# Kernel optimization log

Hardware: AMD Instinct MI355X
Metric: run time of the kernel (lower is better)

The kernel has to match this reference:

```python
import jax, jax.numpy as jnp
import numpy as np

EP = 1e-4
MAX_ITER = 100
L = [512, 512]          # context lengths
C = 256                 # padded feature dim == total_dim
HEADS = 2


def nonsat_activation(x, ep=EP, max_iter=MAX_ITER):
    # Fixed-point iteration y <- (2y^3/3 + x)/(y^2+1), y0 = x.
    # Matches torch version: iterate on detached values, final update uses live x.
    xd = jax.lax.stop_gradient(x)
    f = lambda y: (2.0 * y ** 3 / 3.0 + xd) / (y ** 2 + 1.0)

    def cond(s):
        y, y_new, i = s
        return jnp.logical_and(jnp.mean(jnp.abs(y_new - y)) > ep, i <= max_iter)

    def body(s):
        y, y_new, i = s
        return (y_new, f(y_new), i + 1)

    y_prev, _, _ = jax.lax.while_loop(cond, body, (xd, f(xd), 0))
    y_prev = jax.lax.stop_gradient(y_prev)
    # final (returned) update, differentiable w.r.t. x only
    return (2.0 * y_prev ** 3 / 3.0 + x) / (y_prev ** 2 + 1.0)


def setup_inputs() -> dict:
    key = jax.random.key(0)
    k1, k2, k3 = jax.random.split(key, 3)
    x1 = jax.random.normal(k1, (32, 512, 256), dtype=jnp.float32)
    x2 = jax.random.normal(k2, (32, 512, 192), dtype=jnp.float32)
    # xavier_normal_ for U: std = sqrt(2/(fan_in+fan_out)) = sqrt(2/512) = 1/16
    U = jax.random.normal(k3, (HEADS, C, C), dtype=jnp.float32) * (1.0 / 16.0)
    return {"x1": x1, "x2": x2, "U": U}


def reference(x1, x2, U):
    # pad contexts to common feature dim C (zeros on the right)
    contexts = [x1, jnp.pad(x2, ((0, 0), (0, 0), (0, C - x2.shape[-1])))]
    q = sum(L)
    scaling = C ** (-0.5)
    M = jnp.concatenate(contexts, axis=1)  # (B, q, C)

    # mask uses sizes = L[1:] with blocks starting at offset 0 (faithful quirk)
    mask_mul = jnp.ones((q, q), dtype=jnp.float32).at[:L[1], :L[1]].set(0.0)

    h_reps = []
    mask_add = None
    for h in range(HEADS):
        # K[b,i,j] = sum_{c,d} M[b,i,c] U[h,c,d] M[b,j,d]
        K = jnp.einsum('bic,cd,bjd->bij', M, U[h], M) * scaling
        K = nonsat_activation(K)
        if mask_add is None:  # cached after head 0, reused for later heads
            mask_add = jnp.zeros((q, q), dtype=jnp.float32).at[:L[1], :L[1]].set(jnp.min(K))
        K_hat = K * mask_mul + mask_add
        cols = jnp.max(K_hat, axis=1)   # (B, q) max over rows per column
        rows = jnp.max(K_hat, axis=2)   # (B, q) max over cols per row
        alpha = rows + cols             # (B, q)
        reps = []
        offset = 0
        for i, Ci in enumerate(contexts):
            a = alpha[:, offset:offset + L[i]]          # (B, l_i)
            offset += L[i]
            wt = jax.nn.softmax(a, axis=1)              # (B, l_i)
            r = jnp.einsum('bl,blc->bc', wt, Ci)        # (B, C)
            reps.append(r)
        h_reps.append(jnp.stack(reps, axis=1))          # (B, N, C)
    return jnp.stack(h_reps, axis=0)                    # (heads, B, N, C)
```

## Files before the change

kernel.cpp:

```cpp
#include <hip/hip_runtime.h>
#include <math.h>

typedef _Float16 h16;
typedef h16  h16x8 __attribute__((ext_vector_type(8)));
typedef h16  h16x4 __attribute__((ext_vector_type(4)));
typedef float f32x4 __attribute__((ext_vector_type(4)));

#define MH_OFF   ((size_t)0)
#define ML_OFF   (MH_OFF + 16777216)
#define UHT_OFF  (ML_OFF + 16777216)
#define ULT_OFF  (UHT_OFF + 262144)
#define RMA_OFF  (ULT_OFF + 262144)
#define RMH_OFF  (RMA_OFF + 262144)
#define PCM_OFF  (RMH_OFF + 262144)
#define PMIN_OFF (PCM_OFF + 4194304)
#define M0_OFF   (PMIN_OFF + 4096)
#define AL_OFF   (M0_OFF + 16)

__device__ __forceinline__ void glds16(const void* g, void* l) {
    __builtin_amdgcn_global_load_lds(
        (const __attribute__((address_space(1))) unsigned int*)g,
        (__attribute__((address_space(3))) unsigned int*)l, 16, 0, 0);
}

__device__ __forceinline__ float nonsat(float x) {
    float y = x;
#pragma unroll
    for (int i = 0; i < 24; ++i) {
        float y2 = y * y;
        y = fmaf(0.66666667f * y, y2, x) / (y2 + 1.0f);
    }
    return y;
}

__global__ void k_prep(const float* __restrict__ x1, const float* __restrict__ x2,
                       const float* __restrict__ U, h16* __restrict__ MH,
                       h16* __restrict__ ML, h16* __restrict__ UHt,
                       h16* __restrict__ ULt) {
    const int gid = blockIdx.x * 256 + threadIdx.x;
    if (blockIdx.x < 8192) {
        const int g  = gid;
        const int d4 = (g & 63) * 4;
        const int j  = (g >> 6) & 1023;
        const int b  = g >> 16;
        float v[4];
        if (j < 512) {
            const float* p = x1 + ((size_t)(b * 512 + j) * 256 + d4);
#pragma unroll
            for (int k = 0; k < 4; ++k) v[k] = p[k];
        } else {
            const float* p = x2 + (size_t)(b * 512 + (j - 512)) * 192;
#pragma unroll
            for (int k = 0; k < 4; ++k) {
                const int c = d4 + k;
                v[k] = (c < 192) ? p[c] : 0.0f;
            }
        }
        h16x4 hh, ll;
#pragma unroll
        for (int k = 0; k < 4; ++k) {
            const h16 hi = (h16)v[k];
            hh[k] = hi;
            ll[k] = (h16)(v[k] - (float)hi);
        }
        const size_t o = (size_t)g * 4;
        *(h16x4*)&MH[o] = hh;
        *(h16x4*)&ML[o] = ll;
    } else {
        const int g = gid - 8192 * 256;
        if (g < 32768) {
            const int c4 = (g & 63) * 4;
            const int d  = (g >> 6) & 255;
            const int h  = g >> 14;
            h16x4 hh, ll;
#pragma unroll
            for (int k = 0; k < 4; ++k) {
                const float v = U[((size_t)h * 256 + c4 + k) * 256 + d] * 4.0f;
                const h16 hi = (h16)v;
                hh[k] = hi;
                ll[k] = (h16)(v - (float)hi);
            }
            const size_t o = ((size_t)h * 256 + d) * 256 + c4;
            *(h16x4*)&UHt[o] = hh;
            *(h16x4*)&ULt[o] = ll;
        }
    }
}

__global__ __launch_bounds__(256, 2)
void k_main(const h16* __restrict__ MH, const h16* __restrict__ ML,
            const h16* __restrict__ UHt, const h16* __restrict__ ULt,
            float* __restrict__ rmax_all, float* __restrict__ rmax_hi,
            float* __restrict__ pcm, float* __restrict__ pmin) {
    __shared__ __align__(16) h16 sP[2][64 * 256];
    __shared__ __align__(16) h16 sB[256 * 32];

    const int blk  = blockIdx.x;
    const int rblk = blk & 15;
    const int hb   = blk >> 4;
    const int b    = hb & 31;
    const int h    = hb >> 5;
    const int r0   = rblk * 64;
    const int t    = threadIdx.x;
    const int w    = t >> 6;
    const int l    = t & 63;
    const int q    = l >> 4;
    const int ln   = l & 15;
    const int lrow = l >> 2;
    const int lcol = (l & 3) * 8;

    {
        h16* sA = (h16*)sP;
        f32x4 acc[4][4];
        const f32x4 z4 = {0.f, 0.f, 0.f, 0.f};
#pragma unroll
        for (int i = 0; i < 4; ++i)
#pragma unroll
            for (int j = 0; j < 4; ++j) acc[i][j] = z4;

        for (int ch = 0; ch < 24; ++ch) {
            const int term = ch >> 3;
            const int c0   = (ch & 7) * 32;
            const h16* As = (term == 1) ? ML : MH;
            const h16* Bs = (term == 2) ? ULt : UHt;
            __syncthreads();
            glds16(As + ((size_t)(b * 1024 + r0 + w * 16 + lrow) * 256 + c0 + lcol),
                   &sA[(w * 16) * 32]);
#pragma unroll
            for (int p = 0; p < 4; ++p)
                glds16(Bs + ((size_t)(h * 256 + w * 64 + p * 16 + lrow) * 256 + c0 + lcol),
                       &sB[(w * 64 + p * 16) * 32]);
            __syncthreads();
            h16x8 af[4], bf[4];
#pragma unroll
            for (int ti = 0; ti < 4; ++ti)
                af[ti] = *(const h16x8*)&sA[(ti * 16 + ln) * 32 + q * 8];
#pragma unroll
            for (int tj = 0; tj < 4; ++tj)
                bf[tj] = *(const h16x8*)&sB[(w * 64 + tj * 16 + ln) * 32 + q * 8];
#pragma unroll
            for (int ti = 0; ti < 4; ++ti)
#pragma unroll
                for (int tj = 0; tj < 4; ++tj)
                    acc[ti][tj] = __builtin_amdgcn_mfma_f32_16x16x32_f16(
                        af[ti], bf[tj], acc[ti][tj], 0, 0, 0);
        }
        __syncthreads();
#pragma unroll
        for (int ti = 0; ti < 4; ++ti)
#pragma unroll
            for (int tj = 0; tj < 4; ++tj)
#pragma unroll
                for (int reg = 0; reg < 4; ++reg) {
                    const int r = ti * 16 + q * 4 + reg;
                    const int d = w * 64 + tj * 16 + ln;
                    const float v = acc[ti][tj][reg];
                    const h16 hi = (h16)v;
                    const h16 lo = (h16)(v - (float)hi);
                    const int off = r * 256 + (((d >> 3) ^ (r & 7)) << 3) + (d & 7);
                    sP[0][off] = hi;
                    sP[1][off] = lo;
                }
    }
    __syncthreads();

    float rA[16], rH[16];
#pragma unroll
    for (int i = 0; i < 16; ++i) { rA[i] = -INFINITY; rH[i] = -INFINITY; }
    float gmin = INFINITY;

    for (int jt = 0; jt < 4; ++jt) {
        const int j0 = jt * 256;
        f32x4 acc[4][4];
        const f32x4 z4 = {0.f, 0.f, 0.f, 0.f};
#pragma unroll
        for (int i = 0; i < 4; ++i)
#pragma unroll
            for (int j = 0; j < 4; ++j) acc[i][j] = z4;

        for (int ch = 0; ch < 24; ++ch) {
            const int term = ch >> 3;
            const int kc   = ch & 7;
            const int d0   = kc * 32;
            const h16* Bs  = (term == 2) ? ML : MH;
            const h16* sPs = (term == 1) ? sP[1] : sP[0];
            __syncthreads();
#pragma unroll
            for (int p = 0; p < 4; ++p)
                glds16(Bs + ((size_t)(b * 1024 + j0 + w * 64 + p * 16 + lrow) * 256 + d0 + lcol),
                       &sB[(w * 64 + p * 16) * 32]);
            __syncthreads();
            h16x8 af[4], bf[4];
#pragma unroll
            for (int ti = 0; ti < 4; ++ti) {
                const int r = ti * 16 + ln;
                const int g = (kc * 4 + q) ^ (r & 7);
                af[ti] = *(const h16x8*)&sPs[r * 256 + g * 8];
            }
#pragma unroll
            for (int tj = 0; tj < 4; ++tj)
                bf[tj] = *(const h16x8*)&sB[(w * 64 + tj * 16 + ln) * 32 + q * 8];
#pragma unroll
            for (int ti = 0; ti < 4; ++ti)
#pragma unroll
                for (int tj = 0; tj < 4; ++tj)
                    acc[ti][tj] = __builtin_amdgcn_mfma_f32_16x16x32_f16(
                        af[ti], bf[tj], acc[ti][tj], 0, 0, 0);
        }

        const bool hij = (jt >= 2);
#pragma unroll
        for (int ti = 0; ti < 4; ++ti)
#pragma unroll
            for (int reg = 0; reg < 4; ++reg) {
                float m = acc[ti][0][reg];
                m = fmaxf(m, acc[ti][1][reg]);
                m = fmaxf(m, acc[ti][2][reg]);
                m = fmaxf(m, acc[ti][3][reg]);
                const int idx = ti * 4 + reg;
                rA[idx] = fmaxf(rA[idx], m);
                if (hij) rH[idx] = fmaxf(rH[idx], m);
            }
#pragma unroll
        for (int ti = 0; ti < 4; ++ti)
#pragma unroll
            for (int tj = 0; tj < 4; ++tj)
#pragma unroll
                for (int reg = 0; reg < 4; ++reg)
                    gmin = fminf(gmin, acc[ti][tj][reg]);
#pragma unroll
        for (int tj = 0; tj < 4; ++tj) {
            float m = -INFINITY;
#pragma unroll
            for (int ti = 0; ti < 4; ++ti)
#pragma unroll
                for (int reg = 0; reg < 4; ++reg) m = fmaxf(m, acc[ti][tj][reg]);
            m = fmaxf(m, __shfl_xor(m, 16));
            m = fmaxf(m, __shfl_xor(m, 32));
            if (q == 0)
                pcm[(size_t)(hb * 16 + rblk) * 1024 + j0 + w * 64 + tj * 16 + ln] =
                    m * 0.015625f;
        }
    }

#pragma unroll
    for (int off = 1; off < 64; off <<= 1) gmin = fminf(gmin, __shfl_xor(gmin, off));

    __syncthreads();
    float* red = (float*)sB;
#pragma unroll
    for (int ti = 0; ti < 4; ++ti)
#pragma unroll
        for (int reg = 0; reg < 4; ++reg) {
            const int idx = ti * 4 + reg;
            float a = rA[idx], hh = rH[idx];
#pragma unroll
            for (int o2 = 1; o2 < 16; o2 <<= 1) {
                a  = fmaxf(a,  __shfl_xor(a,  o2));
                hh = fmaxf(hh, __shfl_xor(hh, o2));
            }
            if (ln == 0) {
                const int row = ti * 16 + q * 4 + reg;
                red[w * 64 + row]       = a;
                red[256 + w * 64 + row] = hh;
            }
        }
    if (l == 0) red[512 + w] = gmin;
    __syncthreads();
    if (t < 64) {
        const float a  = fmaxf(fmaxf(red[t], red[64 + t]),
                               fmaxf(red[128 + t], red[192 + t]));
        const float hh = fmaxf(fmaxf(red[256 + t], red[320 + t]),
                               fmaxf(red[384 + t], red[448 + t]));
        rmax_all[(size_t)hb * 1024 + r0 + t] = a * 0.015625f;
        rmax_hi [(size_t)hb * 1024 + r0 + t] = hh * 0.015625f;
    }
    if (t == 0)
        pmin[blk] = fminf(fminf(red[512], red[513]),
                          fminf(red[514], red[515])) * 0.015625f;
}

__global__ void k_min(const float* __restrict__ pmin, float* __restrict__ m0) {
    __shared__ float s[4];
    const int t = threadIdx.x;
    float v = fminf(pmin[t], pmin[t + 256]);
#pragma unroll
    for (int off = 1; off < 64; off <<= 1) v = fminf(v, __shfl_xor(v, off));
    if ((t & 63) == 0) s[t >> 6] = v;
    __syncthreads();
    if (t == 0) m0[0] = fminf(fminf(s[0], s[1]), fminf(s[2], s[3]));
}

__global__ void k_alpha(const float* __restrict__ rmax_all,
                        const float* __restrict__ rmax_hi,
                        const float* __restrict__ pcm,
                        const float* __restrict__ m0p,
                        float* __restrict__ alpha) {
    const int hb = blockIdx.x;
    const float m0 = m0p[0];
    for (int it = 0; it < 4; ++it) {
        const int i = it * 256 + threadIdx.x;
        const float rraw = (i < 512) ? fmaxf(m0, rmax_hi[(size_t)hb * 1024 + i])
                                     : rmax_all[(size_t)hb * 1024 + i];
        float call = -INFINITY, chi = -INFINITY;
#pragma unroll
        for (int rb = 0; rb < 16; ++rb) {
            const float v = pcm[(size_t)(hb * 16 + rb) * 1024 + i];
            call = fmaxf(call, v);
            if (rb >= 8) chi = fmaxf(chi, v);
        }
        const float craw = (i < 512) ? fmaxf(m0, chi) : call;
        alpha[(size_t)hb * 1024 + i] = nonsat(rraw) + nonsat(craw);
    }
}

__global__ __launch_bounds__(256)
void k_out(const float* __restrict__ alpha, const float* __restrict__ x1,
           const float* __restrict__ x2, float* __restrict__ out) {
    __shared__ float wv[512];
    __shared__ float sm[4], ss[4];
    const int blk = blockIdx.x;
    const int seg = blk & 1;
    const int hb  = blk >> 1;
    const int b   = hb & 31;
    const int t   = threadIdx.x;
    const float* ap = alpha + (size_t)hb * 1024 + seg * 512;
    const float a0 = ap[t], a1 = ap[t + 256];

    float m = fmaxf(a0, a1);
#pragma unroll
    for (int off = 1; off < 64; off <<= 1) m = fmaxf(m, __shfl_xor(m, off));
    if ((t & 63) == 0) sm[t >> 6] = m;
    __syncthreads();
    const float amax = fmaxf(fmaxf(sm[0], sm[1]), fmaxf(sm[2], sm[3]));

    const float e0 = __expf(a0 - amax), e1 = __expf(a1 - amax);
    wv[t] = e0; wv[t + 256] = e1;
    float s = e0 + e1;
#pragma unroll
    for (int off = 1; off < 64; off <<= 1) s += __shfl_xor(s, off);
    if ((t & 63) == 0) ss[t >> 6] = s;
    __syncthreads();
    const float inv = 1.0f / (ss[0] + ss[1] + ss[2] + ss[3]);

    float acc = 0.0f;
    if (seg == 0) {
        const float* xp = x1 + (size_t)b * 512 * 256 + t;
#pragma unroll 4
        for (int l = 0; l < 512; ++l) acc = fmaf(wv[l], xp[(size_t)l * 256], acc);
        out[blk * 256 + t] = acc * inv;
    } else {
        if (t < 192) {
            const float* xp = x2 + (size_t)b * 512 * 192 + t;
#pragma unroll 4
            for (int l = 0; l < 512; ++l) acc = fmaf(wv[l], xp[(size_t)l * 192], acc);
            out[blk * 256 + t] = acc * inv;
        } else {
            out[blk * 256 + t] = 0.0f;
        }
    }
}

extern "C" void kernel_launch(void* const* d_in, const int* in_sizes, int n_in,
                              void* d_out, int out_size, void* d_ws, size_t ws_size,
                              hipStream_t stream) {
    const float* x1 = (const float*)d_in[0];
    const float* x2 = (const float*)d_in[1];
    const float* U  = (const float*)d_in[2];
    float* out = (float*)d_out;
    char* wsb  = (char*)d_ws;

    h16*   MHp  = (h16*)(wsb + MH_OFF);
    h16*   MLp  = (h16*)(wsb + ML_OFF);
    h16*   UHt  = (h16*)(wsb + UHT_OFF);
    h16*   ULt  = (h16*)(wsb + ULT_OFF);
    float* rma  = (float*)(wsb + RMA_OFF);
    float* rmh  = (float*)(wsb + RMH_OFF);
    float* pcm  = (float*)(wsb + PCM_OFF);
    float* pmin = (float*)(wsb + PMIN_OFF);
    float* m0   = (float*)(wsb + M0_OFF);
    float* al   = (float*)(wsb + AL_OFF);

    hipLaunchKernelGGL(k_prep,  dim3(8320), dim3(256), 0, stream, x1, x2, U,
                       MHp, MLp, UHt, ULt);
    hipLaunchKernelGGL(k_main,  dim3(1024), dim3(256), 0, stream, MHp, MLp,
                       UHt, ULt, rma, rmh, pcm, pmin);
    hipLaunchKernelGGL(k_min,   dim3(1),    dim3(256), 0, stream, pmin, m0);
    hipLaunchKernelGGL(k_alpha, dim3(64),   dim3(256), 0, stream, rma, rmh, pcm, m0, al);
    hipLaunchKernelGGL(k_out,   dim3(128),  dim3(256), 0, stream, al, x1, x2, out);
}
```

Measured before the change: 315.4 us.

## Load GEMM fragments directly from global, fuse min/alpha into main and output kernels

Both GEMM stages in k_main now load MFMA fragments straight from global memory into registers, without the global-to-LDS staging and the barrier pairs around it. The three split-precision terms now run inside one k-loop. The second GEMM uses wider per-wave tiles (4x8 fragments covering 512 columns per pass), and row maxima are reduced with shuffles into shared memory. The global minimum is computed with an integer-keyed atomicMin, restricted to head 0 blocks, and this replaces the separate k_min kernel. The alpha computation is folded into the output kernel, which removes two launches and an intermediate buffer, at the cost of uncoalesced 16-byte global reads and higher register pressure.

```diff
diff --git a/kernel.cpp b/kernel.cpp
--- a/kernel.cpp
+++ b/kernel.cpp
@@ -13,15 +13,7 @@
 #define RMA_OFF  (ULT_OFF + 262144)
 #define RMH_OFF  (RMA_OFF + 262144)
 #define PCM_OFF  (RMH_OFF + 262144)
-#define PMIN_OFF (PCM_OFF + 4194304)
-#define M0_OFF   (PMIN_OFF + 4096)
-#define AL_OFF   (M0_OFF + 16)
-
-__device__ __forceinline__ void glds16(const void* g, void* l) {
-    __builtin_amdgcn_global_load_lds(
-        (const __attribute__((address_space(1))) unsigned int*)g,
-        (__attribute__((address_space(3))) unsigned int*)l, 16, 0, 0);
-}
+#define M0_OFF   (PCM_OFF + 4194304)
 
 __device__ __forceinline__ float nonsat(float x) {
     float y = x;
@@ -33,10 +25,18 @@
     return y;
 }
 
+__device__ __forceinline__ int fkey(float f) {
+    const int i = __float_as_int(f);
+    return (i >= 0) ? i : (i ^ 0x7fffffff);
+}
+__device__ __forceinline__ float funkey(int k) {
+    return __int_as_float((k >= 0) ? k : (k ^ 0x7fffffff));
+}
+
 __global__ void k_prep(const float* __restrict__ x1, const float* __restrict__ x2,
                        const float* __restrict__ U, h16* __restrict__ MH,
                        h16* __restrict__ ML, h16* __restrict__ UHt,
-                       h16* __restrict__ ULt) {
+                       h16* __restrict__ ULt, int* __restrict__ m0key) {
     const int gid = blockIdx.x * 256 + threadIdx.x;
     if (blockIdx.x < 8192) {
         const int g  = gid;
@@ -83,6 +83,8 @@
             const size_t o = ((size_t)h * 256 + d) * 256 + c4;
             *(h16x4*)&UHt[o] = hh;
             *(h16x4*)&ULt[o] = ll;
+        } else if (g == 32768) {
+            *m0key = 0x7fffffff;
         }
     }
 }
@@ -91,9 +93,9 @@
 void k_main(const h16* __restrict__ MH, const h16* __restrict__ ML,
             const h16* __restrict__ UHt, const h16* __restrict__ ULt,
             float* __restrict__ rmax_all, float* __restrict__ rmax_hi,
-            float* __restrict__ pcm, float* __restrict__ pmin) {
+            float* __restrict__ pcm, int* __restrict__ m0key) {
     __shared__ __align__(16) h16 sP[2][64 * 256];
-    __shared__ __align__(16) h16 sB[256 * 32];
+    __shared__ float red[512 + 4];
 
     const int blk  = blockIdx.x;
     const int rblk = blk & 15;
@@ -106,11 +108,8 @@
     const int l    = t & 63;
     const int q    = l >> 4;
     const int ln   = l & 15;
-    const int lrow = l >> 2;
-    const int lcol = (l & 3) * 8;
 
     {
-        h16* sA = (h16*)sP;
         f32x4 acc[4][4];
         const f32x4 z4 = {0.f, 0.f, 0.f, 0.f};
 #pragma unroll
@@ -118,34 +117,42 @@
 #pragma unroll
             for (int j = 0; j < 4; ++j) acc[i][j] = z4;
 
-        for (int ch = 0; ch < 24; ++ch) {
-            const int term = ch >> 3;
-            const int c0   = (ch & 7) * 32;
-            const h16* As = (term == 1) ? ML : MH;
-            const h16* Bs = (term == 2) ? ULt : UHt;
-            __syncthreads();
-            glds16(As + ((size_t)(b * 1024 + r0 + w * 16 + lrow) * 256 + c0 + lcol),
-                   &sA[(w * 16) * 32]);
-#pragma unroll
-            for (int p = 0; p < 4; ++p)
-                glds16(Bs + ((size_t)(h * 256 + w * 64 + p * 16 + lrow) * 256 + c0 + lcol),
-                       &sB[(w * 64 + p * 16) * 32]);
-            __syncthreads();
-            h16x8 af[4], bf[4];
+        for (int kc = 0; kc < 8; ++kc) {
+            const int c0 = kc * 32;
+            h16x8 aH[4], aL[4], bH[4], bL[4];
+#pragma unroll
+            for (int ti = 0; ti < 4; ++ti) {
+                const size_t off =
+                    (size_t)(b * 1024 + r0 + ti * 16 + ln) * 256 + c0 + q * 8;
+                aH[ti] = *(const h16x8*)&MH[off];
+                aL[ti] = *(const h16x8*)&ML[off];
+            }
+#pragma unroll
+            for (int tj = 0; tj < 4; ++tj) {
+                const size_t off =
+                    (size_t)(h * 256 + w * 64 + tj * 16 + ln) * 256 + c0 + q * 8;
+                bH[tj] = *(const h16x8*)&UHt[off];
+                bL[tj] = *(const h16x8*)&ULt[off];
+            }
 #pragma unroll
             for (int ti = 0; ti < 4; ++ti)
-                af[ti] = *(const h16x8*)&sA[(ti * 16 + ln) * 32 + q * 8];
-#pragma unroll
-            for (int tj = 0; tj < 4; ++tj)
-                bf[tj] = *(const h16x8*)&sB[(w * 64 + tj * 16 + ln) * 32 + q * 8];
+#pragma unroll
+                for (int tj = 0; tj < 4; ++tj)
+                    acc[ti][tj] = __builtin_amdgcn_mfma_f32_16x16x32_f16(
+                        aH[ti], bH[tj], acc[ti][tj], 0, 0, 0);
 #pragma unroll
             for (int ti = 0; ti < 4; ++ti)
 #pragma unroll
                 for (int tj = 0; tj < 4; ++tj)
                     acc[ti][tj] = __builtin_amdgcn_mfma_f32_16x16x32_f16(
-                        af[ti], bf[tj], acc[ti][tj], 0, 0, 0);
-        }
-        __syncthreads();
+                        aL[ti], bH[tj], acc[ti][tj], 0, 0, 0);
+#pragma unroll
+            for (int ti = 0; ti < 4; ++ti)
+#pragma unroll
+                for (int tj = 0; tj < 4; ++tj)
+                    acc[ti][tj] = __builtin_amdgcn_mfma_f32_16x16x32_f16(
+                        aH[ti], bL[tj], acc[ti][tj], 0, 0, 0);
+        }
 #pragma unroll
         for (int ti = 0; ti < 4; ++ti)
 #pragma unroll
@@ -164,72 +171,71 @@
     }
     __syncthreads();
 
-    float rA[16], rH[16];
-#pragma unroll
-    for (int i = 0; i < 16; ++i) { rA[i] = -INFINITY; rH[i] = -INFINITY; }
     float gmin = INFINITY;
 
-    for (int jt = 0; jt < 4; ++jt) {
-        const int j0 = jt * 256;
-        f32x4 acc[4][4];
+    for (int jt = 0; jt < 2; ++jt) {
+        const int jbase = jt * 512 + w * 128;
+        f32x4 acc[4][8];
         const f32x4 z4 = {0.f, 0.f, 0.f, 0.f};
 #pragma unroll
         for (int i = 0; i < 4; ++i)
 #pragma unroll
-            for (int j = 0; j < 4; ++j) acc[i][j] = z4;
-
-        for (int ch = 0; ch < 24; ++ch) {
-            const int term = ch >> 3;
-            const int kc   = ch & 7;
-            const int d0   = kc * 32;
-            const h16* Bs  = (term == 2) ? ML : MH;
-            const h16* sPs = (term == 1) ? sP[1] : sP[0];
-            __syncthreads();
-#pragma unroll
-            for (int p = 0; p < 4; ++p)
-                glds16(Bs + ((size_t)(b * 1024 + j0 + w * 64 + p * 16 + lrow) * 256 + d0 + lcol),
-                       &sB[(w * 64 + p * 16) * 32]);
-            __syncthreads();
-            h16x8 af[4], bf[4];
+            for (int j = 0; j < 8; ++j) acc[i][j] = z4;
+
+        for (int kc = 0; kc < 8; ++kc) {
+            const int d0 = kc * 32;
+            h16x8 aH[4], aL[4], bb[8];
 #pragma unroll
             for (int ti = 0; ti < 4; ++ti) {
                 const int r = ti * 16 + ln;
                 const int g = (kc * 4 + q) ^ (r & 7);
-                af[ti] = *(const h16x8*)&sPs[r * 256 + g * 8];
-            }
-#pragma unroll
-            for (int tj = 0; tj < 4; ++tj)
-                bf[tj] = *(const h16x8*)&sB[(w * 64 + tj * 16 + ln) * 32 + q * 8];
-#pragma unroll
-            for (int ti = 0; ti < 4; ++ti)
-#pragma unroll
-                for (int tj = 0; tj < 4; ++tj)
-                    acc[ti][tj] = __builtin_amdgcn_mfma_f32_16x16x32_f16(
-                        af[ti], bf[tj], acc[ti][tj], 0, 0, 0);
-        }
-
-        const bool hij = (jt >= 2);
+                aH[ti] = *(const h16x8*)&sP[0][r * 256 + g * 8];
+                aL[ti] = *(const h16x8*)&sP[1][r * 256 + g * 8];
+            }
+#pragma unroll
+            for (int tj = 0; tj < 8; ++tj)
+                bb[tj] = *(const h16x8*)&MH[
+                    (size_t)(b * 1024 + jbase + tj * 16 + ln) * 256 + d0 + q * 8];
+#pragma unroll
+            for (int tj = 0; tj < 8; ++tj)
+#pragma unroll
+                for (int ti = 0; ti < 4; ++ti)
+                    acc[ti][tj] = __builtin_amdgcn_mfma_f32_16x16x32_f16(
+                        aH[ti], bb[tj], acc[ti][tj], 0, 0, 0);
+#pragma unroll
+            for (int tj = 0; tj < 8; ++tj)
+#pragma unroll
+                for (int ti = 0; ti < 4; ++ti)
+                    acc[ti][tj] = __builtin_amdgcn_mfma_f32_16x16x32_f16(
+                        aL[ti], bb[tj], acc[ti][tj], 0, 0, 0);
+#pragma unroll
+            for (int tj = 0; tj < 8; ++tj)
+                bb[tj] = *(const h16x8*)&ML[
+                    (size_t)(b * 1024 + jbase + tj * 16 + ln) * 256 + d0 + q * 8];
+#pragma unroll
+            for (int tj = 0; tj < 8; ++tj)
+#pragma unroll
+                for (int ti = 0; ti < 4; ++ti)
+                    acc[ti][tj] = __builtin_amdgcn_mfma_f32_16x16x32_f16(
+                        aH[ti], bb[tj], acc[ti][tj], 0, 0, 0);
+        }
+
 #pragma unroll
         for (int ti = 0; ti < 4; ++ti)
 #pragma unroll
             for (int reg = 0; reg < 4; ++reg) {
                 float m = acc[ti][0][reg];
-                m = fmaxf(m, acc[ti][1][reg]);
-                m = fmaxf(m, acc[ti][2][reg]);
-                m = fmaxf(m, acc[ti][3][reg]);
-                const int idx = ti * 4 + reg;
-                rA[idx] = fmaxf(rA[idx], m);
-                if (hij) rH[idx] = fmaxf(rH[idx], m);
-            }
-#pragma unroll
-        for (int ti = 0; ti < 4; ++ti)
-#pragma unroll
-            for (int tj = 0; tj < 4; ++tj)
-#pragma unroll
-                for (int reg = 0; reg < 4; ++reg)
-                    gmin = fminf(gmin, acc[ti][tj][reg]);
-#pragma unroll
-        for (int tj = 0; tj < 4; ++tj) {
+#pragma unroll
+                for (int tj = 1; tj < 8; ++tj) m = fmaxf(m, acc[ti][tj][reg]);
+                m = fmaxf(m, __shfl_xor(m, 1));
+                m = fmaxf(m, __shfl_xor(m, 2));
+                m = fmaxf(m, __shfl_xor(m, 4));
+                m = fmaxf(m, __shfl_xor(m, 8));
+                if (ln == 0)
+                    red[(jt * 4 + w) * 64 + ti * 16 + q * 4 + reg] = m;
+            }
+#pragma unroll
+        for (int tj = 0; tj < 8; ++tj) {
             float m = -INFINITY;
 #pragma unroll
             for (int ti = 0; ti < 4; ++ti)
@@ -238,85 +244,47 @@
             m = fmaxf(m, __shfl_xor(m, 16));
             m = fmaxf(m, __shfl_xor(m, 32));
             if (q == 0)
-                pcm[(size_t)(hb * 16 + rblk) * 1024 + j0 + w * 64 + tj * 16 + ln] =
+                pcm[(size_t)(hb * 16 + rblk) * 1024 + jbase + tj * 16 + ln] =
                     m * 0.015625f;
         }
+#pragma unroll
+        for (int ti = 0; ti < 4; ++ti)
+#pragma unroll
+            for (int tj = 0; tj < 8; ++tj)
+#pragma unroll
+                for (int reg = 0; reg < 4; ++reg)
+                    gmin = fminf(gmin, acc[ti][tj][reg]);
     }
 
 #pragma unroll
     for (int off = 1; off < 64; off <<= 1) gmin = fminf(gmin, __shfl_xor(gmin, off));
-
-    __syncthreads();
-    float* red = (float*)sB;
-#pragma unroll
-    for (int ti = 0; ti < 4; ++ti)
-#pragma unroll
-        for (int reg = 0; reg < 4; ++reg) {
-            const int idx = ti * 4 + reg;
-            float a = rA[idx], hh = rH[idx];
-#pragma unroll
-            for (int o2 = 1; o2 < 16; o2 <<= 1) {
-                a  = fmaxf(a,  __shfl_xor(a,  o2));
-                hh = fmaxf(hh, __shfl_xor(hh, o2));
-            }
-            if (ln == 0) {
-                const int row = ti * 16 + q * 4 + reg;
-                red[w * 64 + row]       = a;
-                red[256 + w * 64 + row] = hh;
-            }
-        }
     if (l == 0) red[512 + w] = gmin;
     __syncthreads();
+
     if (t < 64) {
-        const float a  = fmaxf(fmaxf(red[t], red[64 + t]),
-                               fmaxf(red[128 + t], red[192 + t]));
-        const float hh = fmaxf(fmaxf(red[256 + t], red[320 + t]),
-                               fmaxf(red[384 + t], red[448 + t]));
-        rmax_all[(size_t)hb * 1024 + r0 + t] = a * 0.015625f;
+        float a = -INFINITY, hh = -INFINITY;
+#pragma unroll
+        for (int w2 = 0; w2 < 4; ++w2) {
+            a  = fmaxf(a,  red[w2 * 64 + t]);
+            const float v1 = red[(4 + w2) * 64 + t];
+            a  = fmaxf(a, v1);
+            hh = fmaxf(hh, v1);
+        }
+        rmax_all[(size_t)hb * 1024 + r0 + t] = a  * 0.015625f;
         rmax_hi [(size_t)hb * 1024 + r0 + t] = hh * 0.015625f;
     }
-    if (t == 0)
-        pmin[blk] = fminf(fminf(red[512], red[513]),
-                          fminf(red[514], red[515])) * 0.015625f;
-}
-
-__global__ void k_min(const float* __restrict__ pmin, float* __restrict__ m0) {
-    __shared__ float s[4];
-    const int t = threadIdx.x;
-    float v = fminf(pmin[t], pmin[t + 256]);
-#pragma unroll
-    for (int off = 1; off < 64; off <<= 1) v = fminf(v, __shfl_xor(v, off));
-    if ((t & 63) == 0) s[t >> 6] = v;
-    __syncthreads();
-    if (t == 0) m0[0] = fminf(fminf(s[0], s[1]), fminf(s[2], s[3]));
-}
-
-__global__ void k_alpha(const float* __restrict__ rmax_all,
-                        const float* __restrict__ rmax_hi,
-                        const float* __restrict__ pcm,
-                        const float* __restrict__ m0p,
-                        float* __restrict__ alpha) {
-    const int hb = blockIdx.x;
-    const float m0 = m0p[0];
-    for (int it = 0; it < 4; ++it) {
-        const int i = it * 256 + threadIdx.x;
-        const float rraw = (i < 512) ? fmaxf(m0, rmax_hi[(size_t)hb * 1024 + i])
-                                     : rmax_all[(size_t)hb * 1024 + i];
-        float call = -INFINITY, chi = -INFINITY;
-#pragma unroll
-        for (int rb = 0; rb < 16; ++rb) {
-            const float v = pcm[(size_t)(hb * 16 + rb) * 1024 + i];
-            call = fmaxf(call, v);
-            if (rb >= 8) chi = fmaxf(chi, v);
-        }
-        const float craw = (i < 512) ? fmaxf(m0, chi) : call;
-        alpha[(size_t)hb * 1024 + i] = nonsat(rraw) + nonsat(craw);
+    if (t == 0 && hb < 32) {
+        const float g4 = fminf(fminf(red[512], red[513]),
+                               fminf(red[514], red[515])) * 0.015625f;
+        atomicMin(m0key, fkey(g4));
     }
 }
 
 __global__ __launch_bounds__(256)
-void k_out(const float* __restrict__ alpha, const float* __restrict__ x1,
-           const float* __restrict__ x2, float* __restrict__ out) {
+void k_fin(const float* __restrict__ rmax_all, const float* __restrict__ rmax_hi,
+           const float* __restrict__ pcm, const int* __restrict__ m0key,
+           const float* __restrict__ x1, const float* __restrict__ x2,
+           float* __restrict__ out) {
     __shared__ float wv[512];
     __shared__ float sm[4], ss[4];
     const int blk = blockIdx.x;
@@ -324,8 +292,26 @@
     const int hb  = blk >> 1;
     const int b   = hb & 31;
     const int t   = threadIdx.x;
-    const float* ap = alpha + (size_t)hb * 1024 + seg * 512;
-    const float a0 = ap[t], a1 = ap[t + 256];
+    const float m0 = funkey(*m0key);
+
+    float a2[2];
+#pragma unroll
+    for (int half = 0; half < 2; ++half) {
+        const int i = seg * 512 + half * 256 + t;
+        float rraw;
+        if (seg == 0) rraw = fmaxf(m0, rmax_hi[(size_t)hb * 1024 + i]);
+        else          rraw = rmax_all[(size_t)hb * 1024 + i];
+        float call = -INFINITY, chi = -INFINITY;
+#pragma unroll
+        for (int rb = 0; rb < 16; ++rb) {
+            const float v = pcm[(size_t)(hb * 16 + rb) * 1024 + i];
+            call = fmaxf(call, v);
+            if (rb >= 8) chi = fmaxf(chi, v);
+        }
+        const float craw = (seg == 0) ? fmaxf(m0, chi) : call;
+        a2[half] = nonsat(rraw) + nonsat(craw);
+    }
+    const float a0 = a2[0], a1 = a2[1];
 
     float m = fmaxf(a0, a1);
 #pragma unroll
@@ -377,15 +363,12 @@
     float* rma  = (float*)(wsb + RMA_OFF);
     float* rmh  = (float*)(wsb + RMH_OFF);
     float* pcm  = (float*)(wsb + PCM_OFF);
-    float* pmin = (float*)(wsb + PMIN_OFF);
-    float* m0   = (float*)(wsb + M0_OFF);
-    float* al   = (float*)(wsb + AL_OFF);
-
-    hipLaunchKernelGGL(k_prep,  dim3(8320), dim3(256), 0, stream, x1, x2, U,
-                       MHp, MLp, UHt, ULt);
-    hipLaunchKernelGGL(k_main,  dim3(1024), dim3(256), 0, stream, MHp, MLp,
-                       UHt, ULt, rma, rmh, pcm, pmin);
-    hipLaunchKernelGGL(k_min,   dim3(1),    dim3(256), 0, stream, pmin, m0);
-    hipLaunchKernelGGL(k_alpha, dim3(64),   dim3(256), 0, stream, rma, rmh, pcm, m0, al);
-    hipLaunchKernelGGL(k_out,   dim3(128),  dim3(256), 0, stream, al, x1, x2, out);
-}
+    int*   m0k  = (int*)(wsb + M0_OFF);
+
+    hipLaunchKernelGGL(k_prep, dim3(8321), dim3(256), 0, stream, x1, x2, U,
+                       MHp, MLp, UHt, ULt, m0k);
+    hipLaunchKernelGGL(k_main, dim3(1024), dim3(256), 0, stream, MHp, MLp,
+                       UHt, ULt, rma, rmh, pcm, m0k);
+    hipLaunchKernelGGL(k_fin,  dim3(128),  dim3(256), 0, stream, rma, rmh,
+                       pcm, m0k, x1, x2, out);
+}
```

After: 307.6 us. -2.5%, faster.
